# Kernel tuning notes

Hardware: AMD Instinct MI355X
Metric: run time of the kernel (lower is better)

The kernel has to match this reference:

```python
import jax, jax.numpy as jnp
import numpy as np

B, LQ, LK, DQ, DK, DV, H = 4, 256, 512, 256, 256, 256, 128


def setup_inputs() -> dict:
    key = jax.random.key(0)
    kq, kk, kv, kwq, kwk, kwv, kl = jax.random.split(key, 7)
    queries = jax.random.normal(kq, (B, LQ, DQ), dtype=jnp.float32)
    keys = jax.random.normal(kk, (B, LK, DK), dtype=jnp.float32)
    values = jax.random.normal(kv, (B, LK, DV), dtype=jnp.float32)
    # Lazy linear params (no bias): W_q: DQ->H, W_k: DK->H, w_v: H->1
    Wq = jax.random.normal(kwq, (DQ, H), dtype=jnp.float32) / np.sqrt(DQ)
    Wk = jax.random.normal(kwk, (DK, H), dtype=jnp.float32) / np.sqrt(DK)
    wv = jax.random.normal(kwv, (H,), dtype=jnp.float32) / np.sqrt(H)
    valid_lens = jax.random.randint(kl, (B,), 1, LK + 1)
    return {"queries": queries, "keys": keys, "values": values,
            "Wq": Wq, "Wk": Wk, "wv": wv, "valid_lens": valid_lens}


def reference(queries, keys, values, Wq, Wk, wv, valid_lens):
    q = jnp.einsum('bqd,dh->bqh', queries, Wq)          # [B,LQ,H]
    k = jnp.einsum('bkd,dh->bkh', keys, Wk)             # [B,LK,H]
    # broadcast-add -> tanh -> reduce over H (the big [B,LQ,LK,H] intermediate)
    features = jnp.tanh(q[:, :, None, :] + k[:, None, :, :])
    scores = jnp.einsum('bqkh,h->bqk', features, wv)    # [B,LQ,LK]
    # masked_softmax with per-batch valid lengths (d2l semantics: masked -> -1e6)
    mask = jnp.arange(scores.shape[-1])[None, None, :] < valid_lens[:, None, None]
    scores = jnp.where(mask, scores, jnp.float32(-1e6))
    attn = jax.nn.softmax(scores, axis=-1)              # [B,LQ,LK]
    return jnp.einsum('bqk,bkv->bqv', attn, values)     # [B,LQ,DV]
```

## Files before the change

### kernel.cpp

```cpp
#include <hip/hip_runtime.h>

#define B_   4
#define LQ_  256
#define LK_  512
#define DQK_ 256
#define DV_  256
#define H_   128

#define TANH_C 2.8853900817779268f
#define L2E    1.4426950408889634f
#define NQBLK (B_ * LQ_ / 4)
#define NKBLK (B_ * LK_ / 4)

__global__ __launch_bounds__(128) void proj_kernel(const float* __restrict__ Q,
                                                   const float* __restrict__ K,
                                                   const float* __restrict__ Wq,
                                                   const float* __restrict__ Wk,
                                                   float* __restrict__ eq,
                                                   float* __restrict__ ekT) {
    const int blk = blockIdx.x;
    const bool isq = blk < NQBLK;
    const float* in = isq ? Q  : K;
    const float* W  = isq ? Wq : Wk;
    const int r0 = (isq ? blk : blk - NQBLK) * 4;
    const int t  = threadIdx.x;

    float acc0 = 0.f, acc1 = 0.f, acc2 = 0.f, acc3 = 0.f;
    const float4* in4 = reinterpret_cast<const float4*>(in + (size_t)r0 * DQK_);
    for (int d4 = 0; d4 < DQK_ / 4; ++d4) {
        float4 r0v = in4[0 * (DQK_ / 4) + d4];
        float4 r1v = in4[1 * (DQK_ / 4) + d4];
        float4 r2v = in4[2 * (DQK_ / 4) + d4];
        float4 r3v = in4[3 * (DQK_ / 4) + d4];
#pragma unroll
        for (int e = 0; e < 4; ++e) {
            float w = W[(size_t)(4 * d4 + e) * H_ + t];
            acc0 = fmaf(reinterpret_cast<const float*>(&r0v)[e], w, acc0);
            acc1 = fmaf(reinterpret_cast<const float*>(&r1v)[e], w, acc1);
            acc2 = fmaf(reinterpret_cast<const float*>(&r2v)[e], w, acc2);
            acc3 = fmaf(reinterpret_cast<const float*>(&r3v)[e], w, acc3);
        }
    }
    float e0 = __builtin_amdgcn_exp2f(acc0 * TANH_C);
    float e1 = __builtin_amdgcn_exp2f(acc1 * TANH_C);
    float e2 = __builtin_amdgcn_exp2f(acc2 * TANH_C);
    float e3 = __builtin_amdgcn_exp2f(acc3 * TANH_C);
    if (isq) {
        eq[(size_t)(r0 + 0) * H_ + t] = e0;
        eq[(size_t)(r0 + 1) * H_ + t] = e1;
        eq[(size_t)(r0 + 2) * H_ + t] = e2;
        eq[(size_t)(r0 + 3) * H_ + t] = e3;
    } else {
        const int b  = r0 >> 9;
        const int k0 = r0 & (LK_ - 1);
        float* o = ekT + ((size_t)(b * H_ + t)) * LK_ + k0;
        *reinterpret_cast<float4*>(o) = make_float4(e0, e1, e2, e3);
    }
}

__global__ __launch_bounds__(1024) void attn_kernel(
    const float* __restrict__ eq,
    const float* __restrict__ ekT,
    const float* __restrict__ wv,
    const float* __restrict__ values,
    const int*   __restrict__ valid_lens,
    float* __restrict__ out) {
    __shared__ float eq_l[4][H_];
    __shared__ float wm2[H_];
    __shared__ float sc[LK_][4];
    __shared__ float part[4][4][DV_];
    __shared__ float red[16];
    __shared__ float inv_s[4];

    const int blk = blockIdx.x;
    const int b   = blk >> 6;
    const int qt  = blk & 63;
    const int t   = threadIdx.x;

    if (t < 512) {
        eq_l[t >> 7][t & 127] = eq[(size_t)(b * LQ_ + qt * 4 + (t >> 7)) * H_ + (t & 127)];
    } else if (t < 640) {
        wm2[t - 512] = -2.f * wv[t - 512];
    }
    __syncthreads();

    const int valid = valid_lens[b];

    {
        const int k    = t & 511;
        const int pair = __builtin_amdgcn_readfirstlane(t >> 9);
        float2 e2 = make_float2(0.f, 0.f);
        if (k < valid) {
            const float* ekp = ekT + (size_t)b * H_ * LK_ + k;
            const float4* w4  = reinterpret_cast<const float4*>(wm2);
            const float4* qa4 = reinterpret_cast<const float4*>(eq_l[2 * pair]);
            const float4* qb4 = reinterpret_cast<const float4*>(eq_l[2 * pair + 1]);
            float p0 = 0.f, p1 = 0.f;
#pragma unroll 4
            for (int h4 = 0; h4 < H_ / 4; ++h4) {
                float4 w  = w4[h4];
                float4 qa = qa4[h4];
                float4 qb = qb4[h4];
#pragma unroll
                for (int e = 0; e < 4; ++e) {
                    float ek = ekp[(size_t)(4 * h4 + e) * LK_];
                    float fa = fmaf(reinterpret_cast<const float*>(&qa)[e], ek, 1.f);
                    float fb = fmaf(reinterpret_cast<const float*>(&qb)[e], ek, 1.f);
                    float ww = reinterpret_cast<const float*>(&w)[e];
                    p0 = fmaf(ww, __builtin_amdgcn_rcpf(fa), p0);
                    p1 = fmaf(ww, __builtin_amdgcn_rcpf(fb), p1);
                }
            }
            e2 = make_float2(__builtin_amdgcn_exp2f(p0 * L2E),
                             __builtin_amdgcn_exp2f(p1 * L2E));
        }
        *reinterpret_cast<float2*>(&sc[k][2 * pair]) = e2;
    }
    __syncthreads();

    const int qi = t >> 8;
    const int kl = t & 255;
    {
        float ss = sc[kl][qi] + sc[kl + 256][qi];
#pragma unroll
        for (int off = 32; off; off >>= 1) ss += __shfl_down(ss, off, 64);
        if ((t & 63) == 0) red[t >> 6] = ss;
    }
    __syncthreads();
    if (t < 4) {
        inv_s[t] = 1.f / (red[4 * t] + red[4 * t + 1] + red[4 * t + 2] + red[4 * t + 3]);
    }
    __syncthreads();

    {
        const int kh = __builtin_amdgcn_readfirstlane(t >> 8);
        const int v  = t & 255;
        const int kstart = kh * 128;
        const int kend   = min(kstart + 128, valid);
        const float* vb = values + (size_t)b * LK_ * DV_ + v;
        float a0 = 0.f, a1 = 0.f, a2 = 0.f, a3 = 0.f;
#pragma unroll 4
        for (int k = kstart; k < kend; ++k) {
            float4 f  = *reinterpret_cast<const float4*>(&sc[k][0]);
            float val = vb[(size_t)k * DV_];
            a0 = fmaf(f.x, val, a0);
            a1 = fmaf(f.y, val, a1);
            a2 = fmaf(f.z, val, a2);
            a3 = fmaf(f.w, val, a3);
        }
        part[kh][0][v] = a0;
        part[kh][1][v] = a1;
        part[kh][2][v] = a2;
        part[kh][3][v] = a3;
    }
    __syncthreads();
    {
        const int v = t & 255;
        float r = (part[0][qi][v] + part[1][qi][v]) + (part[2][qi][v] + part[3][qi][v]);
        out[(size_t)(b * LQ_ + qt * 4 + qi) * DV_ + v] = r * inv_s[qi];
    }
}

extern "C" void kernel_launch(void* const* d_in, const int* in_sizes, int n_in,
                              void* d_out, int out_size, void* d_ws, size_t ws_size,
                              hipStream_t stream) {
    const float* queries    = (const float*)d_in[0];
    const float* keys       = (const float*)d_in[1];
    const float* values     = (const float*)d_in[2];
    const float* Wq         = (const float*)d_in[3];
    const float* Wk         = (const float*)d_in[4];
    const float* wv         = (const float*)d_in[5];
    const int*   valid_lens = (const int*)d_in[6];
    float* out = (float*)d_out;

    float* eq  = (float*)d_ws;
    float* ekT = eq + (size_t)B_ * LQ_ * H_;

    proj_kernel<<<NQBLK + NKBLK, 128, 0, stream>>>(queries, keys, Wq, Wk, eq, ekT);
    attn_kernel<<<B_ * LQ_ / 4, 1024, 0, stream>>>(eq, ekT, wv, values, valid_lens, out);
}
```

Before: 29.98 us.

## Retile score and PV stages into register tiles with split-H reduction

The score stage now gives each thread a 4-key by 4-query register tile over a 16-wide slice of H. It loads the keys with a float4 read and reuses each loaded ek across four queries. Partial sums go to a shared scratch buffer and are reduced over 8 H-slices before the exp. The PV stage now uses float4 value loads with 4x4 register tiles, split into 16 key chunks, followed by a 16-way shared reduction. This reduces global ekT and values traffic per FLOP, at the cost of more shared memory, extra reduction passes and higher register use.

New measurement: 28.97 us. -3.4%, faster.

```diff
diff --git a/kernel.cpp b/kernel.cpp
--- a/kernel.cpp
+++ b/kernel.cpp
@@ -68,9 +68,12 @@
     __shared__ float eq_l[4][H_];
     __shared__ float wm2[H_];
     __shared__ float sc[LK_][4];
-    __shared__ float part[4][4][DV_];
+    __shared__ float scratch[8 * 128 * 20];
     __shared__ float red[16];
     __shared__ float inv_s[4];
+
+    float (*partB)[128][20] = reinterpret_cast<float (*)[128][20]>(scratch);
+    float (*partD)[4][DV_]  = reinterpret_cast<float (*)[4][DV_]>(scratch);
 
     const int blk = blockIdx.x;
     const int b   = blk >> 6;
@@ -87,34 +90,47 @@
     const int valid = valid_lens[b];
 
     {
-        const int k    = t & 511;
-        const int pair = __builtin_amdgcn_readfirstlane(t >> 9);
-        float2 e2 = make_float2(0.f, 0.f);
-        if (k < valid) {
-            const float* ekp = ekT + (size_t)b * H_ * LK_ + k;
-            const float4* w4  = reinterpret_cast<const float4*>(wm2);
-            const float4* qa4 = reinterpret_cast<const float4*>(eq_l[2 * pair]);
-            const float4* qb4 = reinterpret_cast<const float4*>(eq_l[2 * pair + 1]);
-            float p0 = 0.f, p1 = 0.f;
-#pragma unroll 4
-            for (int h4 = 0; h4 < H_ / 4; ++h4) {
-                float4 w  = w4[h4];
-                float4 qa = qa4[h4];
-                float4 qb = qb4[h4];
-#pragma unroll
-                for (int e = 0; e < 4; ++e) {
-                    float ek = ekp[(size_t)(4 * h4 + e) * LK_];
-                    float fa = fmaf(reinterpret_cast<const float*>(&qa)[e], ek, 1.f);
-                    float fb = fmaf(reinterpret_cast<const float*>(&qb)[e], ek, 1.f);
-                    float ww = reinterpret_cast<const float*>(&w)[e];
-                    p0 = fmaf(ww, __builtin_amdgcn_rcpf(fa), p0);
-                    p1 = fmaf(ww, __builtin_amdgcn_rcpf(fb), p1);
+        const int quad = t & 127;
+        const int hs   = t >> 7;
+        const int k0   = 4 * quad;
+        float acc[16];
+#pragma unroll
+        for (int i = 0; i < 16; ++i) acc[i] = 0.f;
+
+        if (k0 < valid) {
+            const float* ekb = ekT + (size_t)b * H_ * LK_ + k0;
+#pragma unroll 2
+            for (int hh = 0; hh < 16; ++hh) {
+                const int h = 16 * hs + hh;
+                float4 ek = *reinterpret_cast<const float4*>(ekb + (size_t)h * LK_);
+                float w = wm2[h];
+#pragma unroll
+                for (int r = 0; r < 4; ++r) {
+                    float qv = eq_l[r][h];
+                    acc[4 * r + 0] = fmaf(w, __builtin_amdgcn_rcpf(fmaf(qv, ek.x, 1.f)), acc[4 * r + 0]);
+                    acc[4 * r + 1] = fmaf(w, __builtin_amdgcn_rcpf(fmaf(qv, ek.y, 1.f)), acc[4 * r + 1]);
+                    acc[4 * r + 2] = fmaf(w, __builtin_amdgcn_rcpf(fmaf(qv, ek.z, 1.f)), acc[4 * r + 2]);
+                    acc[4 * r + 3] = fmaf(w, __builtin_amdgcn_rcpf(fmaf(qv, ek.w, 1.f)), acc[4 * r + 3]);
                 }
             }
-            e2 = make_float2(__builtin_amdgcn_exp2f(p0 * L2E),
-                             __builtin_amdgcn_exp2f(p1 * L2E));
         }
-        *reinterpret_cast<float2*>(&sc[k][2 * pair]) = e2;
+        float* pb = &partB[hs][quad][0];
+#pragma unroll
+        for (int i = 0; i < 4; ++i)
+            *reinterpret_cast<float4*>(pb + 4 * i) = *reinterpret_cast<float4*>(&acc[4 * i]);
+    }
+    __syncthreads();
+
+#pragma unroll
+    for (int j = 0; j < 2; ++j) {
+        const int o    = t + 1024 * j;
+        const int quad = o >> 4;
+        const int idx  = o & 15;
+        const int k    = 4 * quad + (idx & 3);
+        float s = 0.f;
+#pragma unroll
+        for (int hs = 0; hs < 8; ++hs) s += partB[hs][quad][idx];
+        sc[k][idx >> 2] = (k < valid) ? __builtin_amdgcn_exp2f(s * L2E) : 0.f;
     }
     __syncthreads();
 
@@ -133,31 +149,39 @@
     __syncthreads();
 
     {
-        const int kh = __builtin_amdgcn_readfirstlane(t >> 8);
-        const int v  = t & 255;
-        const int kstart = kh * 128;
-        const int kend   = min(kstart + 128, valid);
+        const int w  = __builtin_amdgcn_readfirstlane(t >> 6);
+        const int v  = 4 * (t & 63);
+        const int kstart = 32 * w;
+        const int kend   = min(kstart + 32, valid);
         const float* vb = values + (size_t)b * LK_ * DV_ + v;
-        float a0 = 0.f, a1 = 0.f, a2 = 0.f, a3 = 0.f;
-#pragma unroll 4
+        float4 a0 = make_float4(0.f, 0.f, 0.f, 0.f);
+        float4 a1 = a0, a2 = a0, a3 = a0;
+#pragma unroll 2
         for (int k = kstart; k < kend; ++k) {
-            float4 f  = *reinterpret_cast<const float4*>(&sc[k][0]);
-            float val = vb[(size_t)k * DV_];
-            a0 = fmaf(f.x, val, a0);
-            a1 = fmaf(f.y, val, a1);
-            a2 = fmaf(f.z, val, a2);
-            a3 = fmaf(f.w, val, a3);
+            float4 sv = *reinterpret_cast<const float4*>(&sc[k][0]);
+            float4 vv = *reinterpret_cast<const float4*>(vb + (size_t)k * DV_);
+            a0.x = fmaf(sv.x, vv.x, a0.x); a0.y = fmaf(sv.x, vv.y, a0.y);
+            a0.z = fmaf(sv.x, vv.z, a0.z); a0.w = fmaf(sv.x, vv.w, a0.w);
+            a1.x = fmaf(sv.y, vv.x, a1.x); a1.y = fmaf(sv.y, vv.y, a1.y);
+            a1.z = fmaf(sv.y, vv.z, a1.z); a1.w = fmaf(sv.y, vv.w, a1.w);
+            a2.x = fmaf(sv.z, vv.x, a2.x); a2.y = fmaf(sv.z, vv.y, a2.y);
+            a2.z = fmaf(sv.z, vv.z, a2.z); a2.w = fmaf(sv.z, vv.w, a2.w);
+            a3.x = fmaf(sv.w, vv.x, a3.x); a3.y = fmaf(sv.w, vv.y, a3.y);
+            a3.z = fmaf(sv.w, vv.z, a3.z); a3.w = fmaf(sv.w, vv.w, a3.w);
         }
-        part[kh][0][v] = a0;
-        part[kh][1][v] = a1;
-        part[kh][2][v] = a2;
-        part[kh][3][v] = a3;
-    }
-    __syncthreads();
-    {
+        *reinterpret_cast<float4*>(&partD[w][0][v]) = a0;
+        *reinterpret_cast<float4*>(&partD[w][1][v]) = a1;
+        *reinterpret_cast<float4*>(&partD[w][2][v]) = a2;
+        *reinterpret_cast<float4*>(&partD[w][3][v]) = a3;
+    }
+    __syncthreads();
+    {
+        const int r = t >> 8;
         const int v = t & 255;
-        float r = (part[0][qi][v] + part[1][qi][v]) + (part[2][qi][v] + part[3][qi][v]);
-        out[(size_t)(b * LQ_ + qt * 4 + qi) * DV_ + v] = r * inv_s[qi];
+        float s = 0.f;
+#pragma unroll
+        for (int w = 0; w < 16; ++w) s += partD[w][r][v];
+        out[(size_t)(b * LQ_ + qt * 4 + r) * DV_ + v] = s * inv_s[r];
     }
 }
 
```
